# Kernel optimization log

Hardware: AMD Instinct MI355X
Metric: run time of the kernel (lower is better)

The kernel has to match this reference:

```python
import jax, jax.numpy as jnp
import numpy as np

NH = 12  # num_heads

def setup_inputs() -> dict:
    key = jax.random.key(0)
    ks = jax.random.split(key, 8)
    B, N, C = 8, 1024, 768
    d = C // NH  # head_dim == qk_head_dim (qk_head_dim=None)
    s = 0.02
    return {
        "x": jax.random.normal(ks[0], (B, N, C), jnp.float32),
        "Wq": jax.random.normal(ks[1], (C, NH * d), jnp.float32) * s,
        "Wk": jax.random.normal(ks[2], (C, NH * d), jnp.float32) * s,
        "Wv": jax.random.normal(ks[3], (C, C), jnp.float32) * s,
        "Wproj": jax.random.normal(ks[4], (C, C), jnp.float32) * s,
        "proj_b": jax.random.normal(ks[5], (C,), jnp.float32) * s,
        "attn_bias": jax.random.normal(ks[6], (N, N), jnp.float32) * s,
        "head_bias": jax.random.normal(ks[7], (NH, N, N), jnp.float32) * s,
    }

def reference(x, Wq, Wk, Wv, Wproj, proj_b, attn_bias, head_bias):
    B, N, C = x.shape
    d = C // NH
    scale = d ** -0.5
    # projections: [B,N,C] -> [B,nh,N,d]
    q = jnp.einsum('bnc,ce->bne', x, Wq).reshape(B, N, NH, d).transpose(0, 2, 1, 3)
    k = jnp.einsum('bnc,ce->bne', x, Wk).reshape(B, N, NH, d).transpose(0, 2, 1, 3)
    v = jnp.einsum('bnc,ce->bne', x, Wv).reshape(B, N, NH, d).transpose(0, 2, 1, 3)
    # scaled scores + global bias + per-head bias
    scores = jnp.einsum('bhnd,bhmd->bhnm', q * scale, k)
    scores = scores + attn_bias[None, None] + head_bias[None]
    attn = jax.nn.softmax(scores, axis=-1)  # [B,nh,N,N]
    out = jnp.einsum('bhnm,bhmd->bhnd', attn, v)
    out = out.transpose(0, 2, 1, 3).reshape(B, N, C)
    out = jnp.einsum('bnc,ce->bne', out, Wproj) + proj_b
    return out, attn
```

## Files before the change

### kernel.cpp

```cpp
#include <hip/hip_runtime.h>
#include <hip/hip_bf16.h>
#include <cstddef>

#define B_   8
#define N_   1024
#define C_   768
#define NH_  12
#define HD_  64
#define M_   (B_ * N_)

typedef __attribute__((ext_vector_type(8))) short  short8;
typedef __attribute__((ext_vector_type(4))) float  f32x4;

__device__ __forceinline__ unsigned short f2b(float f) {
    union { float f; unsigned u; } v; v.f = f;
    unsigned u = v.u;
    return (unsigned short)((u + 0x7FFFu + ((u >> 16) & 1u)) >> 16);
}
__device__ __forceinline__ float b2f(unsigned short s) {
    union { unsigned u; float f; } v; v.u = ((unsigned)s) << 16;
    return v.f;
}
__device__ __forceinline__ ushort2 pk2(float a, float b) {
    __hip_bfloat162 t = __float22bfloat162_rn(make_float2(a, b));
    return *(ushort2*)&t;
}
__device__ __forceinline__ void gld16(const unsigned short* g, unsigned short* l) {
    __builtin_amdgcn_global_load_lds(
        (const __attribute__((address_space(1))) void*)g,
        (__attribute__((address_space(3))) void*)l, 16, 0, 0);
}

__global__ __launch_bounds__(256) void prepass_kernel(
    const float* __restrict__ x,
    const float* __restrict__ w0, const float* __restrict__ w1,
    const float* __restrict__ w2, const float* __restrict__ w3,
    const float* __restrict__ ab, const float* __restrict__ hbias,
    unsigned short* __restrict__ xb,
    unsigned short* __restrict__ t0, unsigned short* __restrict__ t1,
    unsigned short* __restrict__ t2, unsigned short* __restrict__ t3,
    unsigned short* __restrict__ bc) {
    const int bid = blockIdx.x;
    if (bid < 2304) {
        const int z = bid / 576, t = bid % 576;
        const float* src = (z == 0) ? w0 : (z == 1) ? w1 : (z == 2) ? w2 : w3;
        unsigned short* dst = (z == 0) ? t0 : (z == 1) ? t1 : (z == 2) ? t2 : t3;
        __shared__ float tile[32][33];
        const int r0 = (t / 24) * 32, c0 = (t % 24) * 32;
        const int tx = threadIdx.x & 31, ty = threadIdx.x >> 5;
        #pragma unroll
        for (int p = 0; p < 4; ++p)
            tile[ty + 8 * p][tx] = src[(size_t)(r0 + ty + 8 * p) * C_ + c0 + tx];
        __syncthreads();
        #pragma unroll
        for (int p = 0; p < 4; ++p)
            dst[(size_t)(c0 + ty + 8 * p) * C_ + r0 + tx] = f2b(tile[tx][ty + 8 * p]);
    } else {
        const int castN4 = M_ * C_ / 4;
        const int biasN4 = NH_ * N_ * N_ / 4;
        const int qm4 = N_ * N_ / 4;
        const int stride = (4096 - 2304) * 256;
        for (int i = (bid - 2304) * 256 + threadIdx.x; i < castN4 + biasN4; i += stride) {
            if (i < castN4) {
                float4 v = ((const float4*)x)[i];
                ushort2 lo = pk2(v.x, v.y), hi = pk2(v.z, v.w);
                ushort4 o; o.x = lo.x; o.y = lo.y; o.z = hi.x; o.w = hi.y;
                ((ushort4*)xb)[i] = o;
            } else {
                int j = i - castN4;
                float4 a = ((const float4*)ab)[j % qm4];
                float4 h = ((const float4*)hbias)[j];
                ushort2 lo = pk2(a.x + h.x, a.y + h.y), hi = pk2(a.z + h.z, a.w + h.w);
                ushort4 o; o.x = lo.x; o.y = lo.y; o.z = hi.x; o.w = hi.y;
                ((ushort4*)bc)[j] = o;
            }
        }
    }
}

__global__ __launch_bounds__(256) void qkv_gemm(
    const unsigned short* __restrict__ A,
    const unsigned short* __restrict__ W0, const unsigned short* __restrict__ W1,
    const unsigned short* __restrict__ W2,
    unsigned short* __restrict__ o0, unsigned short* __restrict__ o1,
    unsigned short* __restrict__ o2) {
    __shared__ unsigned short As[128 * 32];
    __shared__ unsigned short Bs[128 * 32];
    const int z = blockIdx.z;
    const unsigned short* Bt = (z == 0) ? W0 : (z == 1) ? W1 : W2;
    const int tid = threadIdx.x;
    const int wid = tid >> 6, lane = tid & 63;
    const int ln = lane & 15, g = lane >> 4;
    const int wm = wid >> 1, wn = wid & 1;
    const int bm = blockIdx.y * 128, bn = blockIdx.x * 128;
    const int lrow = lane >> 2, lch = (lane & 3) * 8;

    f32x4 acc[4][4];
    #pragma unroll
    for (int i = 0; i < 4; ++i)
        #pragma unroll
        for (int j = 0; j < 4; ++j) acc[i][j] = (f32x4)0.f;

    for (int k0 = 0; k0 < C_; k0 += 32) {
        #pragma unroll
        for (int p = 0; p < 2; ++p) {
            const int rowbase = (wid + p * 4) * 16;
            gld16(&A [(size_t)(bm + rowbase + lrow) * C_ + k0 + lch], &As[rowbase * 32]);
            gld16(&Bt[(size_t)(bn + rowbase + lrow) * C_ + k0 + lch], &Bs[rowbase * 32]);
        }
        __syncthreads();
        short8 a[4], b[4];
        #pragma unroll
        for (int mt = 0; mt < 4; ++mt)
            a[mt] = *(const short8*)&As[(wm * 64 + mt * 16 + ln) * 32 + g * 8];
        #pragma unroll
        for (int nt = 0; nt < 4; ++nt)
            b[nt] = *(const short8*)&Bs[(wn * 64 + nt * 16 + ln) * 32 + g * 8];
        #pragma unroll
        for (int mt = 0; mt < 4; ++mt)
            #pragma unroll
            for (int nt = 0; nt < 4; ++nt)
                acc[mt][nt] = __builtin_amdgcn_mfma_f32_16x16x32_bf16(
                    a[mt], b[nt], acc[mt][nt], 0, 0, 0);
        __syncthreads();
    }

    unsigned short* outp = (z == 0) ? o0 : (z == 1) ? o1 : o2;
    #pragma unroll
    for (int mt = 0; mt < 4; ++mt) {
        #pragma unroll
        for (int nt = 0; nt < 4; ++nt) {
            f32x4 c = acc[mt][nt];
            int rowb = bm + wm * 64 + mt * 16 + g * 4;
            int col  = bn + wn * 64 + nt * 16 + ln;
            int hh = col >> 6, dd = col & 63;
            if (z < 2) {
                #pragma unroll
                for (int i = 0; i < 4; ++i) {
                    int row = rowb + i;
                    int bb = row >> 10, n = row & 1023;
                    outp[((size_t)(bb * NH_ + hh) * N_ + n) * HD_ + dd] = f2b(c[i]);
                }
            } else {
                int bb = rowb >> 10, n0 = rowb & 1023;
                ushort2 lo = pk2(c[0], c[1]), hi = pk2(c[2], c[3]);
                ushort4 pk; pk.x = lo.x; pk.y = lo.y; pk.z = hi.x; pk.w = hi.y;
                *(ushort4*)&outp[((size_t)(bb * NH_ + hh) * HD_ + dd) * N_ + n0] = pk;
            }
        }
    }
}

__global__ __launch_bounds__(256) void proj_gemm(
    const unsigned short* __restrict__ A, const unsigned short* __restrict__ Bt,
    const float* __restrict__ bias, float* __restrict__ outp) {
    __shared__ unsigned short As[128 * 32];
    __shared__ unsigned short Bs[128 * 32];
    const int tid = threadIdx.x;
    const int wid = tid >> 6, lane = tid & 63;
    const int ln = lane & 15, g = lane >> 4;
    const int wm = wid >> 1, wn = wid & 1;
    const int bm = blockIdx.y * 128, bn = blockIdx.x * 128;
    const int lrow = lane >> 2, lch = (lane & 3) * 8;

    f32x4 acc[4][4];
    #pragma unroll
    for (int i = 0; i < 4; ++i)
        #pragma unroll
        for (int j = 0; j < 4; ++j) acc[i][j] = (f32x4)0.f;

    for (int k0 = 0; k0 < C_; k0 += 32) {
        #pragma unroll
        for (int p = 0; p < 2; ++p) {
            const int rowbase = (wid + p * 4) * 16;
            gld16(&A [(size_t)(bm + rowbase + lrow) * C_ + k0 + lch], &As[rowbase * 32]);
            gld16(&Bt[(size_t)(bn + rowbase + lrow) * C_ + k0 + lch], &Bs[rowbase * 32]);
        }
        __syncthreads();
        short8 a[4], b[4];
        #pragma unroll
        for (int mt = 0; mt < 4; ++mt)
            a[mt] = *(const short8*)&As[(wm * 64 + mt * 16 + ln) * 32 + g * 8];
        #pragma unroll
        for (int nt = 0; nt < 4; ++nt)
            b[nt] = *(const short8*)&Bs[(wn * 64 + nt * 16 + ln) * 32 + g * 8];
        #pragma unroll
        for (int mt = 0; mt < 4; ++mt)
            #pragma unroll
            for (int nt = 0; nt < 4; ++nt)
                acc[mt][nt] = __builtin_amdgcn_mfma_f32_16x16x32_bf16(
                    a[mt], b[nt], acc[mt][nt], 0, 0, 0);
        __syncthreads();
    }

    #pragma unroll
    for (int mt = 0; mt < 4; ++mt) {
        #pragma unroll
        for (int nt = 0; nt < 4; ++nt) {
            f32x4 c = acc[mt][nt];
            int rowb = bm + wm * 64 + mt * 16 + g * 4;
            int col  = bn + wn * 64 + nt * 16 + ln;
            float bb = bias[col];
            #pragma unroll
            for (int i = 0; i < 4; ++i)
                outp[(size_t)(rowb + i) * C_ + col] = c[i] + bb;
        }
    }
}

__global__ __launch_bounds__(512, 4) void attn_fused(
    const unsigned short* __restrict__ qh, const unsigned short* __restrict__ kh,
    const unsigned short* __restrict__ vt,
    const unsigned short* __restrict__ bias_c,
    float* __restrict__ attn_out, unsigned short* __restrict__ hb) {
    __shared__ unsigned short sc[32 * 1024];
    __shared__ float sinv[32];
    const int id = blockIdx.x;
    const int xcd = id & 7;
    const int b = (id >> 3) & 7;
    const int qbh = ((id >> 6) << 3) + xcd;
    const int qb0 = (qbh / NH_) * 32;
    const int h = qbh % NH_;
    const int bh = b * NH_ + h;
    const int tid = threadIdx.x;
    const int wid = tid >> 6, lane = tid & 63;
    const int ln = lane & 15, g = lane >> 4;

    #define SCP(row, m) ((unsigned short*)((char*)sc + (row) * 2048 + \
                         (((m) * 2) ^ (((row) & 7) << 4))))

    {
        short8 qf[2][2];
        #pragma unroll
        for (int Mt = 0; Mt < 2; ++Mt)
            #pragma unroll
            for (int kc = 0; kc < 2; ++kc)
                qf[Mt][kc] = *(const short8*)&qh[
                    ((size_t)bh * N_ + qb0 + Mt * 16 + ln) * HD_ + kc * 32 + g * 8];
        const int mb = wid * 128;
        const unsigned short* kbase = kh + (size_t)bh * N_ * HD_;
        short8 k0 = *(const short8*)&kbase[(size_t)(mb + ln) * HD_ + g * 8];
        short8 k1 = *(const short8*)&kbase[(size_t)(mb + ln) * HD_ + 32 + g * 8];
        for (int mt = 0; mt < 8; ++mt) {
            const int m0 = mb + mt * 16;
            const int m1 = (mt < 7) ? m0 + 16 : m0;
            short8 n0 = *(const short8*)&kbase[(size_t)(m1 + ln) * HD_ + g * 8];
            short8 n1 = *(const short8*)&kbase[(size_t)(m1 + ln) * HD_ + 32 + g * 8];
            #pragma unroll
            for (int Mt = 0; Mt < 2; ++Mt) {
                f32x4 s = (f32x4)0.f;
                s = __builtin_amdgcn_mfma_f32_16x16x32_bf16(k0, qf[Mt][0], s, 0, 0, 0);
                s = __builtin_amdgcn_mfma_f32_16x16x32_bf16(k1, qf[Mt][1], s, 0, 0, 0);
                const int mrow = m0 + g * 4;
                ushort2 lo = pk2(s[0] * 0.125f, s[1] * 0.125f);
                ushort2 hi = pk2(s[2] * 0.125f, s[3] * 0.125f);
                ushort4 pk; pk.x = lo.x; pk.y = lo.y; pk.z = hi.x; pk.w = hi.y;
                *(ushort4*)SCP(Mt * 16 + ln, mrow) = pk;
            }
            k0 = n0; k1 = n1;
        }
    }
    __syncthreads();

    f32x4 sv[16];
    const int r2 = tid >> 4, t16 = tid & 15;
    {
        const unsigned short* brow = bias_c + ((size_t)h * N_ + qb0 + r2) * N_;
        float mx = -1e30f;
        #pragma unroll
        for (int j = 0; j < 16; ++j) {
            ushort4 er = *(const ushort4*)SCP(r2, t16 * 4 + j * 64);
            ushort4 bb = *(const ushort4*)&brow[t16 * 4 + j * 64];
            sv[j][0] = b2f(er.x) + b2f(bb.x);
            sv[j][1] = b2f(er.y) + b2f(bb.y);
            sv[j][2] = b2f(er.z) + b2f(bb.z);
            sv[j][3] = b2f(er.w) + b2f(bb.w);
            mx = fmaxf(fmaxf(fmaxf(mx, sv[j][0]), fmaxf(sv[j][1], sv[j][2])), sv[j][3]);
        }
        #pragma unroll
        for (int off = 8; off; off >>= 1) mx = fmaxf(mx, __shfl_xor(mx, off, 16));
        float sum = 0.f;
        #pragma unroll
        for (int j = 0; j < 16; ++j) {
            float e0 = __expf(sv[j][0] - mx);
            float e1 = __expf(sv[j][1] - mx);
            float e2 = __expf(sv[j][2] - mx);
            float e3 = __expf(sv[j][3] - mx);
            sv[j][0] = e0; sv[j][1] = e1; sv[j][2] = e2; sv[j][3] = e3;
            sum += (e0 + e1) + (e2 + e3);
            ushort2 lo = pk2(e0, e1), hi = pk2(e2, e3);
            ushort4 pk; pk.x = lo.x; pk.y = lo.y; pk.z = hi.x; pk.w = hi.y;
            *(ushort4*)SCP(r2, t16 * 4 + j * 64) = pk;
        }
        #pragma unroll
        for (int off = 8; off; off >>= 1) sum += __shfl_xor(sum, off, 16);
        if (t16 == 0) sinv[r2] = 1.f / sum;
    }
    __syncthreads();

    {
        const float invr = sinv[r2];
        float* arow = attn_out + ((size_t)bh * N_ + qb0 + r2) * N_ + t16 * 4;
        const int Mt = wid >> 2, nt = wid & 3;
        const unsigned short* vrow = vt + ((size_t)bh * HD_ + nt * 16 + ln) * N_;
        f32x4 acc = (f32x4)0.f;
        short8 pa = *(const short8*)SCP(Mt * 16 + ln, g * 8);
        short8 vb = *(const short8*)&vrow[g * 8];
        #pragma unroll
        for (int kt2 = 0; kt2 < 16; ++kt2) {
            {
                const int kn = 2 * kt2 + 1;
                short8 npa = *(const short8*)SCP(Mt * 16 + ln, kn * 32 + g * 8);
                short8 nvb = *(const short8*)&vrow[kn * 32 + g * 8];
                acc = __builtin_amdgcn_mfma_f32_16x16x32_bf16(pa, vb, acc, 0, 0, 0);
                pa = npa; vb = nvb;
            }
            {
                f32x4 o;
                o[0] = sv[kt2][0] * invr; o[1] = sv[kt2][1] * invr;
                o[2] = sv[kt2][2] * invr; o[3] = sv[kt2][3] * invr;
                __builtin_nontemporal_store(o, (f32x4*)&arow[kt2 * 64]);
            }
            {
                const int kn = (kt2 < 15) ? 2 * kt2 + 2 : 2 * kt2 + 1;
                short8 npa = *(const short8*)SCP(Mt * 16 + ln, kn * 32 + g * 8);
                short8 nvb = *(const short8*)&vrow[kn * 32 + g * 8];
                acc = __builtin_amdgcn_mfma_f32_16x16x32_bf16(pa, vb, acc, 0, 0, 0);
                pa = npa; vb = nvb;
            }
        }
        #pragma unroll
        for (int i = 0; i < 4; ++i) {
            int q = qb0 + Mt * 16 + g * 4 + i;
            float o = acc[i] * sinv[Mt * 16 + g * 4 + i];
            hb[(size_t)((b << 10) + q) * C_ + h * HD_ + nt * 16 + ln] = f2b(o);
        }
    }
    #undef SCP
}

extern "C" void kernel_launch(void* const* d_in, const int* in_sizes, int n_in,
                              void* d_out, int out_size, void* d_ws, size_t ws_size,
                              hipStream_t stream) {
    const float* x         = (const float*)d_in[0];
    const float* Wq        = (const float*)d_in[1];
    const float* Wk        = (const float*)d_in[2];
    const float* Wv        = (const float*)d_in[3];
    const float* Wproj     = (const float*)d_in[4];
    const float* proj_b    = (const float*)d_in[5];
    const float* attn_bias = (const float*)d_in[6];
    const float* head_bias = (const float*)d_in[7];

    float* out  = (float*)d_out;
    float* attn = out + (size_t)B_ * N_ * C_;

    unsigned short* ws = (unsigned short*)d_ws;
    const size_t SZ_X = (size_t)M_ * C_;
    const size_t SZ_W = (size_t)C_ * C_;
    unsigned short* xb  = ws;
    unsigned short* wqt = xb + SZ_X;
    unsigned short* wkt = wqt + SZ_W;
    unsigned short* wvt = wkt + SZ_W;
    unsigned short* wpt = wvt + SZ_W;
    unsigned short* qh  = wpt + SZ_W;
    unsigned short* khd = qh + SZ_X;
    unsigned short* vtp = khd + SZ_X;
    unsigned short* bc  = vtp + SZ_X;
    unsigned short* hb  = xb;

    prepass_kernel<<<4096, 256, 0, stream>>>(
        x, Wq, Wk, Wv, Wproj, attn_bias, head_bias,
        xb, wqt, wkt, wvt, wpt, bc);

    qkv_gemm<<<dim3(C_ / 128, M_ / 128, 3), 256, 0, stream>>>(
        xb, wqt, wkt, wvt, qh, khd, vtp);

    attn_fused<<<dim3(B_ * (N_ / 32) * NH_), 512, 0, stream>>>(
        qh, khd, vtp, bc, attn, hb);

    proj_gemm<<<dim3(C_ / 128, M_ / 128), 256, 0, stream>>>(hb, wpt, proj_b, out);
}
```

Measured before the change: 292.9 us.

## Reuse bias rows across batches and double-buffer QK^T scores in attention

Each block now handles a 16-query tile of one head for four batches in turn, so it loads the same bias row slice four times in a row from a warm cache. The QK^T scores for the next batch are computed into a second LDS buffer while softmax and PV run on the current one. PV is split over the key dimension between two wave halves and reduced through LDS. The cost is one extra barrier per batch, a smaller M tile per MFMA pass, and dropping the XCD-aware block ordering and the occupancy hint in launch_bounds.

```diff
diff --git a/kernel.cpp b/kernel.cpp
--- a/kernel.cpp
+++ b/kernel.cpp
@@ -208,132 +208,142 @@
     }
 }
 
-__global__ __launch_bounds__(512, 4) void attn_fused(
+__global__ __launch_bounds__(512) void attn_fused(
     const unsigned short* __restrict__ qh, const unsigned short* __restrict__ kh,
     const unsigned short* __restrict__ vt,
     const unsigned short* __restrict__ bias_c,
     float* __restrict__ attn_out, unsigned short* __restrict__ hb) {
-    __shared__ unsigned short sc[32 * 1024];
-    __shared__ float sinv[32];
+    __shared__ unsigned short sc[2][16 * 1024];
+    __shared__ f32x4 red[4][64];
+    __shared__ float sinv[16];
     const int id = blockIdx.x;
-    const int xcd = id & 7;
-    const int b = (id >> 3) & 7;
-    const int qbh = ((id >> 6) << 3) + xcd;
-    const int qb0 = (qbh / NH_) * 32;
+    const int bp = id & 1;
+    const int qbh = id >> 1;
+    const int qb0 = (qbh / NH_) * 16;
     const int h = qbh % NH_;
-    const int bh = b * NH_ + h;
     const int tid = threadIdx.x;
     const int wid = tid >> 6, lane = tid & 63;
     const int ln = lane & 15, g = lane >> 4;
 
-    #define SCP(row, m) ((unsigned short*)((char*)sc + (row) * 2048 + \
-                         (((m) * 2) ^ (((row) & 7) << 4))))
-
-    {
-        short8 qf[2][2];
-        #pragma unroll
-        for (int Mt = 0; Mt < 2; ++Mt)
-            #pragma unroll
-            for (int kc = 0; kc < 2; ++kc)
-                qf[Mt][kc] = *(const short8*)&qh[
-                    ((size_t)bh * N_ + qb0 + Mt * 16 + ln) * HD_ + kc * 32 + g * 8];
+    #define SCP(bufi, row, m) ((unsigned short*)((char*)sc[bufi] + (row) * 2048 + \
+                               (((m) * 2) ^ (((row) & 7) << 4))))
+
+    auto qkt = [&](int b, int bufi) {
+        const int bh = b * NH_ + h;
+        short8 qf0 = *(const short8*)&qh[((size_t)bh * N_ + qb0 + ln) * HD_ + g * 8];
+        short8 qf1 = *(const short8*)&qh[((size_t)bh * N_ + qb0 + ln) * HD_ + 32 + g * 8];
+        const unsigned short* kbase = kh + (size_t)bh * N_ * HD_;
         const int mb = wid * 128;
-        const unsigned short* kbase = kh + (size_t)bh * N_ * HD_;
         short8 k0 = *(const short8*)&kbase[(size_t)(mb + ln) * HD_ + g * 8];
         short8 k1 = *(const short8*)&kbase[(size_t)(mb + ln) * HD_ + 32 + g * 8];
+        #pragma unroll
         for (int mt = 0; mt < 8; ++mt) {
             const int m0 = mb + mt * 16;
             const int m1 = (mt < 7) ? m0 + 16 : m0;
             short8 n0 = *(const short8*)&kbase[(size_t)(m1 + ln) * HD_ + g * 8];
             short8 n1 = *(const short8*)&kbase[(size_t)(m1 + ln) * HD_ + 32 + g * 8];
-            #pragma unroll
-            for (int Mt = 0; Mt < 2; ++Mt) {
-                f32x4 s = (f32x4)0.f;
-                s = __builtin_amdgcn_mfma_f32_16x16x32_bf16(k0, qf[Mt][0], s, 0, 0, 0);
-                s = __builtin_amdgcn_mfma_f32_16x16x32_bf16(k1, qf[Mt][1], s, 0, 0, 0);
-                const int mrow = m0 + g * 4;
-                ushort2 lo = pk2(s[0] * 0.125f, s[1] * 0.125f);
-                ushort2 hi = pk2(s[2] * 0.125f, s[3] * 0.125f);
-                ushort4 pk; pk.x = lo.x; pk.y = lo.y; pk.z = hi.x; pk.w = hi.y;
-                *(ushort4*)SCP(Mt * 16 + ln, mrow) = pk;
-            }
+            f32x4 s = (f32x4)0.f;
+            s = __builtin_amdgcn_mfma_f32_16x16x32_bf16(k0, qf0, s, 0, 0, 0);
+            s = __builtin_amdgcn_mfma_f32_16x16x32_bf16(k1, qf1, s, 0, 0, 0);
+            const int mrow = m0 + g * 4;
+            ushort2 lo = pk2(s[0] * 0.125f, s[1] * 0.125f);
+            ushort2 hi = pk2(s[2] * 0.125f, s[3] * 0.125f);
+            ushort4 pk; pk.x = lo.x; pk.y = lo.y; pk.z = hi.x; pk.w = hi.y;
+            *(ushort4*)SCP(bufi, ln, mrow) = pk;
             k0 = n0; k1 = n1;
         }
-    }
-    __syncthreads();
-
-    f32x4 sv[16];
-    const int r2 = tid >> 4, t16 = tid & 15;
-    {
-        const unsigned short* brow = bias_c + ((size_t)h * N_ + qb0 + r2) * N_;
-        float mx = -1e30f;
-        #pragma unroll
-        for (int j = 0; j < 16; ++j) {
-            ushort4 er = *(const ushort4*)SCP(r2, t16 * 4 + j * 64);
-            ushort4 bb = *(const ushort4*)&brow[t16 * 4 + j * 64];
-            sv[j][0] = b2f(er.x) + b2f(bb.x);
-            sv[j][1] = b2f(er.y) + b2f(bb.y);
-            sv[j][2] = b2f(er.z) + b2f(bb.z);
-            sv[j][3] = b2f(er.w) + b2f(bb.w);
-            mx = fmaxf(fmaxf(fmaxf(mx, sv[j][0]), fmaxf(sv[j][1], sv[j][2])), sv[j][3]);
-        }
-        #pragma unroll
-        for (int off = 8; off; off >>= 1) mx = fmaxf(mx, __shfl_xor(mx, off, 16));
-        float sum = 0.f;
-        #pragma unroll
-        for (int j = 0; j < 16; ++j) {
-            float e0 = __expf(sv[j][0] - mx);
-            float e1 = __expf(sv[j][1] - mx);
-            float e2 = __expf(sv[j][2] - mx);
-            float e3 = __expf(sv[j][3] - mx);
-            sv[j][0] = e0; sv[j][1] = e1; sv[j][2] = e2; sv[j][3] = e3;
-            sum += (e0 + e1) + (e2 + e3);
-            ushort2 lo = pk2(e0, e1), hi = pk2(e2, e3);
-            ushort4 pk; pk.x = lo.x; pk.y = lo.y; pk.z = hi.x; pk.w = hi.y;
-            *(ushort4*)SCP(r2, t16 * 4 + j * 64) = pk;
-        }
-        #pragma unroll
-        for (int off = 8; off; off >>= 1) sum += __shfl_xor(sum, off, 16);
-        if (t16 == 0) sinv[r2] = 1.f / sum;
-    }
-    __syncthreads();
-
-    {
-        const float invr = sinv[r2];
-        float* arow = attn_out + ((size_t)bh * N_ + qb0 + r2) * N_ + t16 * 4;
-        const int Mt = wid >> 2, nt = wid & 3;
-        const unsigned short* vrow = vt + ((size_t)bh * HD_ + nt * 16 + ln) * N_;
-        f32x4 acc = (f32x4)0.f;
-        short8 pa = *(const short8*)SCP(Mt * 16 + ln, g * 8);
-        short8 vb = *(const short8*)&vrow[g * 8];
-        #pragma unroll
-        for (int kt2 = 0; kt2 < 16; ++kt2) {
-            {
-                const int kn = 2 * kt2 + 1;
-                short8 npa = *(const short8*)SCP(Mt * 16 + ln, kn * 32 + g * 8);
+    };
+
+    qkt(bp * 4, 0);
+
+    for (int i = 0; i < 4; ++i) {
+        const int b = bp * 4 + i;
+        const int bufi = i & 1;
+        __syncthreads();
+
+        if (i < 3) qkt(b + 1, bufi ^ 1);
+
+        const int r2 = tid >> 5, t32 = tid & 31;
+        {
+            const unsigned short* brow = bias_c + ((size_t)h * N_ + qb0 + r2) * N_;
+            float sv[4][8];
+            float mx = -1e30f;
+            #pragma unroll
+            for (int j = 0; j < 4; ++j) {
+                const int m = t32 * 8 + j * 256;
+                short8 er = *(const short8*)SCP(bufi, r2, m);
+                short8 bb = *(const short8*)&brow[m];
+                #pragma unroll
+                for (int e = 0; e < 8; ++e) {
+                    sv[j][e] = b2f((unsigned short)er[e]) + b2f((unsigned short)bb[e]);
+                    mx = fmaxf(mx, sv[j][e]);
+                }
+            }
+            #pragma unroll
+            for (int off = 16; off; off >>= 1) mx = fmaxf(mx, __shfl_xor(mx, off, 32));
+            float sum = 0.f;
+            #pragma unroll
+            for (int j = 0; j < 4; ++j) {
+                #pragma unroll
+                for (int e = 0; e < 8; ++e) {
+                    sv[j][e] = __expf(sv[j][e] - mx);
+                    sum += sv[j][e];
+                }
+                ushort2 p0 = pk2(sv[j][0], sv[j][1]);
+                ushort2 p1 = pk2(sv[j][2], sv[j][3]);
+                ushort2 p2 = pk2(sv[j][4], sv[j][5]);
+                ushort2 p3 = pk2(sv[j][6], sv[j][7]);
+                short8 pk;
+                pk[0] = p0.x; pk[1] = p0.y; pk[2] = p1.x; pk[3] = p1.y;
+                pk[4] = p2.x; pk[5] = p2.y; pk[6] = p3.x; pk[7] = p3.y;
+                *(short8*)SCP(bufi, r2, t32 * 8 + j * 256) = pk;
+            }
+            #pragma unroll
+            for (int off = 16; off; off >>= 1) sum += __shfl_xor(sum, off, 32);
+            const float inv = 1.f / sum;
+            if (t32 == 0) sinv[r2] = inv;
+            float* arow = attn_out + (((size_t)(b * NH_ + h) * N_) + qb0 + r2) * N_ + t32 * 8;
+            #pragma unroll
+            for (int j = 0; j < 4; ++j) {
+                f32x4 o0, o1;
+                o0[0] = sv[j][0] * inv; o0[1] = sv[j][1] * inv;
+                o0[2] = sv[j][2] * inv; o0[3] = sv[j][3] * inv;
+                o1[0] = sv[j][4] * inv; o1[1] = sv[j][5] * inv;
+                o1[2] = sv[j][6] * inv; o1[3] = sv[j][7] * inv;
+                __builtin_nontemporal_store(o0, (f32x4*)&arow[j * 256]);
+                __builtin_nontemporal_store(o1, (f32x4*)&arow[j * 256 + 4]);
+            }
+        }
+        __syncthreads();
+
+        {
+            const int nt = wid & 3, khf = wid >> 2;
+            const unsigned short* vrow =
+                vt + ((size_t)(b * NH_ + h) * HD_ + nt * 16 + ln) * N_;
+            f32x4 acc = (f32x4)0.f;
+            const int kb0 = khf * 16;
+            short8 pa = *(const short8*)SCP(bufi, ln, kb0 * 32 + g * 8);
+            short8 vb = *(const short8*)&vrow[kb0 * 32 + g * 8];
+            #pragma unroll
+            for (int kt = 0; kt < 16; ++kt) {
+                const int kn = kb0 + ((kt < 15) ? kt + 1 : kt);
+                short8 npa = *(const short8*)SCP(bufi, ln, kn * 32 + g * 8);
                 short8 nvb = *(const short8*)&vrow[kn * 32 + g * 8];
                 acc = __builtin_amdgcn_mfma_f32_16x16x32_bf16(pa, vb, acc, 0, 0, 0);
                 pa = npa; vb = nvb;
             }
-            {
-                f32x4 o;
-                o[0] = sv[kt2][0] * invr; o[1] = sv[kt2][1] * invr;
-                o[2] = sv[kt2][2] * invr; o[3] = sv[kt2][3] * invr;
-                __builtin_nontemporal_store(o, (f32x4*)&arow[kt2 * 64]);
-            }
-            {
-                const int kn = (kt2 < 15) ? 2 * kt2 + 2 : 2 * kt2 + 1;
-                short8 npa = *(const short8*)SCP(Mt * 16 + ln, kn * 32 + g * 8);
-                short8 nvb = *(const short8*)&vrow[kn * 32 + g * 8];
-                acc = __builtin_amdgcn_mfma_f32_16x16x32_bf16(pa, vb, acc, 0, 0, 0);
-                pa = npa; vb = nvb;
-            }
-        }
-        #pragma unroll
-        for (int i = 0; i < 4; ++i) {
-            int q = qb0 + Mt * 16 + g * 4 + i;
-            float o = acc[i] * sinv[Mt * 16 + g * 4 + i];
-            hb[(size_t)((b << 10) + q) * C_ + h * HD_ + nt * 16 + ln] = f2b(o);
+            if (khf == 1) red[nt][lane] = acc;
+            __syncthreads();
+            if (khf == 0) {
+                acc += red[nt][lane];
+                const int col = h * HD_ + nt * 16 + ln;
+                #pragma unroll
+                for (int i2 = 0; i2 < 4; ++i2) {
+                    int q = qb0 + g * 4 + i2;
+                    hb[(size_t)((b << 10) + q) * C_ + col] =
+                        f2b(acc[i2] * sinv[g * 4 + i2]);
+                }
+            }
         }
     }
     #undef SCP
@@ -375,7 +385,7 @@
     qkv_gemm<<<dim3(C_ / 128, M_ / 128, 3), 256, 0, stream>>>(
         xb, wqt, wkt, wvt, qh, khd, vtp);
 
-    attn_fused<<<dim3(B_ * (N_ / 32) * NH_), 512, 0, stream>>>(
+    attn_fused<<<dim3(1536), 512, 0, stream>>>(
         qh, khd, vtp, bc, attn, hb);
 
     proj_gemm<<<dim3(C_ / 128, M_ / 128), 256, 0, stream>>>(hb, wpt, proj_b, out);
```

Result: slower. 362.8 us (+23.8%).
